# Kernel optimization log

Hardware: AMD Instinct MI355X
Metric: run time of the kernel (lower is better)

Reference implementation:

```python
import jax, jax.numpy as jnp
import numpy as np

C_CURV = 1.0  # hyperbolic curvature (init kwarg c)
EPS = 1e-7


def _to_ball(v, max_norm=0.8):
    # rescale rows to lie strictly inside the unit Poincare ball
    n = jnp.linalg.norm(v, axis=-1, keepdims=True)
    return v * (max_norm / (n + 1.0))


def setup_inputs() -> dict:
    key = jax.random.key(0)
    k1, k2 = jax.random.split(key)
    B, C, D = 32768, 2048, 512
    z_mix = _to_ball(jax.random.normal(k1, (B, D), dtype=jnp.float32))
    prototypes = _to_ball(jax.random.normal(k2, (C, D), dtype=jnp.float32))
    repel_margin = jnp.float32(2.0)
    return {"z_mix": z_mix, "prototypes": prototypes, "repel_margin": repel_margin}


def dist_matrix(x, y, c):
    # Poincare-ball pairwise distance (arccosh form):
    # d(x,y) = arccosh(1 + 2c||x-y||^2 / ((1-c||x||^2)(1-c||y||^2))) / sqrt(c)
    x2 = jnp.sum(x * x, axis=-1)            # (B,)
    y2 = jnp.sum(y * y, axis=-1)            # (C,)
    xy = jnp.einsum('bd,cd->bc', x, y)      # (B, C)
    sqdist = jnp.maximum(x2[:, None] + y2[None, :] - 2.0 * xy, 0.0)
    denom = (1.0 - c * x2)[:, None] * (1.0 - c * y2)[None, :]
    arg = 1.0 + 2.0 * c * sqdist / jnp.maximum(denom, EPS)
    return jnp.arccosh(jnp.maximum(arg, 1.0 + EPS)) / jnp.sqrt(c)


def reference(z_mix, prototypes, repel_margin):
    dist2proto = dist_matrix(z_mix, prototypes, C_CURV)   # (B, C)
    min_dist = jnp.min(dist2proto, axis=1)                # (B,)
    return jnp.mean(jax.nn.relu(repel_margin - min_dist))
```

## Files before the change

kernel.cpp:

```cpp
#include <hip/hip_runtime.h>
#include <stdint.h>

#define EPS_F 1e-7f

typedef float f32x4 __attribute__((ext_vector_type(4)));
typedef int   v8i   __attribute__((ext_vector_type(8)));

union A32 { uint4 u4[2]; v8i v; };

__device__ __forceinline__ unsigned cvt4(float a, float b, float c, float d) {
  int v = __builtin_amdgcn_cvt_pk_fp8_f32(a, b, 0, false);
  return (unsigned)__builtin_amdgcn_cvt_pk_fp8_f32(c, d, v, true);
}

#define MFMA128(A, B, C) __builtin_amdgcn_mfma_scale_f32_16x16x128_f8f6f4( \
    (A), (B), (C), 0, 0, 0, 0x7F7F7F7F, 0, 0x7F7F7F7F)


__global__ __launch_bounds__(256) void prep_kernel(
    const float* __restrict__ protos, uint8_t* __restrict__ wsB,
    float* __restrict__ y2a, float* __restrict__ rya,
    float* __restrict__ out) {
  const int lane = threadIdx.x & 63;
  const int w    = threadIdx.x >> 6;
  const int c    = blockIdx.x * 4 + w;
  const int g    = c >> 4, cl = c & 15;
  const float4* p = (const float4*)(protos + (size_t)c * 512 + lane * 8);
  float4 f0 = p[0], f1 = p[1];
  float s = f0.x*f0.x + f0.y*f0.y + f0.z*f0.z + f0.w*f0.w
          + f1.x*f1.x + f1.y*f1.y + f1.z*f1.z + f1.w*f1.w;
#pragma unroll
  for (int off = 32; off > 0; off >>= 1) s += __shfl_xor(s, off, 64);
  if (lane == 0) { y2a[c] = s; rya[c] = 1.f / (1.f - s); }
  unsigned ux = cvt4(f0.x, f0.y, f0.z, f0.w);
  unsigned uy = cvt4(f1.x, f1.y, f1.z, f1.w);
  const int kb = lane >> 4, kg = (lane >> 2) & 3, bo = lane & 3;
  size_t ri  = (size_t)(g * 4 + kb) * 64 + kg * 16 + cl;
  size_t off = ri * 16 + (size_t)(bo & 1) * 8 + (size_t)(bo >> 1) * (512u * 1024u);
  *(uint2*)(wsB + off) = make_uint2(ux, uy);
  if (blockIdx.x == 0 && threadIdx.x == 0) out[0] = 0.f;
}

__global__ __launch_bounds__(512, 1) void gemm_min_kernel(
    const float* __restrict__ z, const uint8_t* __restrict__ wsB,
    const float* __restrict__ y2a, const float* __restrict__ rya,
    const float* __restrict__ marg, float* __restrict__ out) {
  __shared__ uint4 As2[2048];
  __shared__ float x2s[64];
  __shared__ float rxs[64];
  __shared__ float minbuf[64][8];

  const int tid  = threadIdx.x;
  const int lane = tid & 63;
  const int w    = tid >> 6;
  const int q    = lane >> 4;
  const int l15  = lane & 15;
  const size_t rowbase = (size_t)blockIdx.x * 64;

  const uint4* BLo = (const uint4*)wsB;
  const uint4* BHi = BLo + 32768;

  A32 Bp0[2], Bp1[2];
#pragma unroll
  for (int i = 0; i < 2; ++i) {
    size_t r0 = (size_t)(w * 64 + i) * 64 + lane;
    Bp0[i].u4[0] = BLo[r0];       Bp0[i].u4[1] = BHi[r0];
    Bp1[i].u4[0] = BLo[r0 + 256]; Bp1[i].u4[1] = BHi[r0 + 256];
  }

  {
    const int c4 = lane & 3;
    const int m  = lane >> 2;
    const float* zb = z + (rowbase + w * 8) * 512 + lane * 4;
    float p0 = 0.f, p1 = 0.f, p2 = 0.f, p3 = 0.f,
          p4 = 0.f, p5 = 0.f, p6 = 0.f, p7 = 0.f;
#pragma unroll
    for (int ss = 0; ss < 4; ++ss) {
      float4 f0 = *(const float4*)(zb + (2 * ss + 0) * 512);
      float4 f1 = *(const float4*)(zb + (2 * ss + 0) * 512 + 256);
      float4 f2 = *(const float4*)(zb + (2 * ss + 1) * 512);
      float4 f3 = *(const float4*)(zb + (2 * ss + 1) * 512 + 256);
      float sa = f0.x*f0.x + f0.y*f0.y + f0.z*f0.z + f0.w*f0.w
               + f1.x*f1.x + f1.y*f1.y + f1.z*f1.z + f1.w*f1.w;
      float sb = f2.x*f2.x + f2.y*f2.y + f2.z*f2.z + f2.w*f2.w
               + f3.x*f3.x + f3.y*f3.y + f3.z*f3.z + f3.w*f3.w;
      if (ss == 0) { p0 += sa; p1 += sb; }
      if (ss == 1) { p2 += sa; p3 += sb; }
      if (ss == 2) { p4 += sa; p5 += sb; }
      if (ss == 3) { p6 += sa; p7 += sb; }
      unsigned v0 = cvt4(f0.x, f0.y, f0.z, f0.w);
      unsigned v1 = cvt4(f1.x, f1.y, f1.z, f1.w);
      unsigned v2 = cvt4(f2.x, f2.y, f2.z, f2.w);
      unsigned v3 = cvt4(f3.x, f3.y, f3.z, f3.w);
      unsigned t;
      t = (unsigned)__shfl_xor((int)((c4 & 1) ? v0 : v1), 1, 64);
      if (c4 & 1) v0 = t; else v1 = t;
      t = (unsigned)__shfl_xor((int)((c4 & 1) ? v2 : v3), 1, 64);
      if (c4 & 1) v2 = t; else v3 = t;
      t = (unsigned)__shfl_xor((int)((c4 & 2) ? v0 : v2), 2, 64);
      if (c4 & 2) v0 = t; else v2 = t;
      t = (unsigned)__shfl_xor((int)((c4 & 2) ? v1 : v3), 2, 64);
      if (c4 & 2) v1 = t; else v3 = t;
      int K   = ((c4 & 1) << 8) + (m << 4);
      int kb  = K >> 7;
      int kg  = (K >> 5) & 3;
      int pl  = (K >> 4) & 1;
      int r15 = ((w & 1) << 3) + 2 * ss + (c4 >> 1);
      int rf  = w >> 1;
      int ri  = pl * 1024 + (kb * 4 + rf) * 64 + kg * 16 + r15;
      As2[ri] = make_uint4(v0, v1, v2, v3);
    }
    float pr[8] = {p0, p1, p2, p3, p4, p5, p6, p7};
#pragma unroll
    for (int i = 0; i < 8; ++i) {
      float v = pr[i];
#pragma unroll
      for (int off = 32; off > 0; off >>= 1) v += __shfl_xor(v, off, 64);
      if (lane == 0) { x2s[w * 8 + i] = v; rxs[w * 8 + i] = 1.f / (1.f - v); }
    }
  }
  __syncthreads();

  float x2r[4][4];
#pragma unroll
  for (int rf = 0; rf < 4; ++rf) {
    float4 x4 = *(const float4*)&x2s[rf * 16 + q * 4];
    x2r[rf][0] = x4.x; x2r[rf][1] = x4.y; x2r[rf][2] = x4.z; x2r[rf][3] = x4.w;
  }

  float tmin[4][4];
#pragma unroll
  for (int rf = 0; rf < 4; ++rf)
#pragma unroll
    for (int r = 0; r < 4; ++r) tmin[rf][r] = 3.4e38f;

  const float* y2p = y2a + w * 256 + l15;
  const float* ryp = rya + w * 256 + l15;

#pragma clang loop unroll(disable)
  for (int s = 0; s < 8; ++s) {
    f32x4 acc[4][2];
#pragma unroll
    for (int rf = 0; rf < 4; ++rf) {
      f32x4 z4 = {0.f, 0.f, 0.f, 0.f};
      acc[rf][0] = z4; acc[rf][1] = z4;
    }
    float y2v0 = y2p[s * 32],      ryv0 = ryp[s * 32];
    float y2v1 = y2p[s * 32 + 16], ryv1 = ryp[s * 32 + 16];

#pragma unroll
    for (int kb = 0; kb < 4; ++kb) {
#pragma unroll
      for (int rf = 0; rf < 4; ++rf) {
        A32 a;
        int ri = (kb * 4 + rf) * 64 + lane;
        a.u4[0] = As2[ri];
        a.u4[1] = As2[1024 + ri];
        acc[rf][0] = MFMA128(a.v, Bp0[kb & 1].v, acc[rf][0]);
        acc[rf][1] = MFMA128(a.v, Bp1[kb & 1].v, acc[rf][1]);
      }
      {
        int ip = s * 4 + kb + 2;
        size_t r0 = (size_t)(w * 64 + (ip >> 2) * 8 + (ip & 3)) * 64 + lane;
        Bp0[kb & 1].u4[0] = BLo[r0];       Bp0[kb & 1].u4[1] = BHi[r0];
        Bp1[kb & 1].u4[0] = BLo[r0 + 256]; Bp1[kb & 1].u4[1] = BHi[r0 + 256];
      }
    }

#pragma unroll
    for (int rf = 0; rf < 4; ++rf) {
#pragma unroll
      for (int r = 0; r < 4; ++r) {
        float xv = x2r[rf][r];
        float u0 = fmaxf(fmaf(-2.f, acc[rf][0][r], xv + y2v0), 0.f) * ryv0;
        float u1 = fmaxf(fmaf(-2.f, acc[rf][1][r], xv + y2v1), 0.f) * ryv1;
        tmin[rf][r] = fminf(tmin[rf][r], fminf(u0, u1));
      }
    }
  }

#pragma unroll
  for (int rf = 0; rf < 4; ++rf) {
#pragma unroll
    for (int r = 0; r < 4; ++r) {
      float v = tmin[rf][r];
      v = fminf(v, __shfl_xor(v, 1, 64));
      v = fminf(v, __shfl_xor(v, 2, 64));
      v = fminf(v, __shfl_xor(v, 4, 64));
      v = fminf(v, __shfl_xor(v, 8, 64));
      if (l15 == 0) minbuf[rf * 16 + q * 4 + r][w] = v;
    }
  }
  __syncthreads();

  if (w == 0) {
    float m = minbuf[lane][0];
#pragma unroll
    for (int i = 1; i < 8; ++i) m = fminf(m, minbuf[lane][i]);
    float t = m * rxs[lane];
    float arg = fmaxf(fmaf(2.f, t, 1.f), 1.f + EPS_F);
    float contrib = fmaxf(marg[0] - acoshf(arg), 0.f);
#pragma unroll
    for (int off = 32; off > 0; off >>= 1) contrib += __shfl_xor(contrib, off, 64);
    if (lane == 0) atomicAdd(out, contrib * (1.0f / 32768.f));
  }
}

extern "C" void kernel_launch(void* const* d_in, const int* in_sizes, int n_in,
                              void* d_out, int out_size, void* d_ws, size_t ws_size,
                              hipStream_t stream) {
  const float* z      = (const float*)d_in[0];
  const float* protos = (const float*)d_in[1];
  const float* marg   = (const float*)d_in[2];
  float* out = (float*)d_out;
  uint8_t* wsB = (uint8_t*)d_ws;
  float* y2a = (float*)((char*)d_ws + (1 << 20) + 192 * 1024);
  float* rya = y2a + 2048;

  prep_kernel<<<512, 256, 0, stream>>>(protos, wsB, y2a, rya, out);
  gemm_min_kernel<<<512, 512, 0, stream>>>(z, wsB, y2a, rya, marg, out);
}
```

Measured before the change: 135.3 us.

## Double row tile per block to 128 and halve waves per block

```diff
diff --git a/kernel.cpp b/kernel.cpp
--- a/kernel.cpp
+++ b/kernel.cpp
@@ -41,21 +41,21 @@
   if (blockIdx.x == 0 && threadIdx.x == 0) out[0] = 0.f;
 }
 
-__global__ __launch_bounds__(512, 1) void gemm_min_kernel(
+__global__ __launch_bounds__(256, 1) void gemm_min_kernel(
     const float* __restrict__ z, const uint8_t* __restrict__ wsB,
     const float* __restrict__ y2a, const float* __restrict__ rya,
     const float* __restrict__ marg, float* __restrict__ out) {
-  __shared__ uint4 As2[2048];
-  __shared__ float x2s[64];
-  __shared__ float rxs[64];
-  __shared__ float minbuf[64][8];
+  __shared__ uint4 As2[4096];
+  __shared__ float x2s[128];
+  __shared__ float rxs[128];
+  __shared__ float minbuf[128][4];
 
   const int tid  = threadIdx.x;
   const int lane = tid & 63;
   const int w    = tid >> 6;
   const int q    = lane >> 4;
   const int l15  = lane & 15;
-  const size_t rowbase = (size_t)blockIdx.x * 64;
+  const size_t rowbase = (size_t)blockIdx.x * 128;
 
   const uint4* BLo = (const uint4*)wsB;
   const uint4* BHi = BLo + 32768;
@@ -63,7 +63,7 @@
   A32 Bp0[2], Bp1[2];
 #pragma unroll
   for (int i = 0; i < 2; ++i) {
-    size_t r0 = (size_t)(w * 64 + i) * 64 + lane;
+    size_t r0 = (size_t)(w * 128 + i) * 64 + lane;
     Bp0[i].u4[0] = BLo[r0];       Bp0[i].u4[1] = BHi[r0];
     Bp1[i].u4[0] = BLo[r0 + 256]; Bp1[i].u4[1] = BHi[r0 + 256];
   }
@@ -71,11 +71,9 @@
   {
     const int c4 = lane & 3;
     const int m  = lane >> 2;
-    const float* zb = z + (rowbase + w * 8) * 512 + lane * 4;
-    float p0 = 0.f, p1 = 0.f, p2 = 0.f, p3 = 0.f,
-          p4 = 0.f, p5 = 0.f, p6 = 0.f, p7 = 0.f;
-#pragma unroll
-    for (int ss = 0; ss < 4; ++ss) {
+    const float* zb = z + (rowbase + w * 32) * 512 + lane * 4;
+#pragma unroll
+    for (int ss = 0; ss < 16; ++ss) {
       float4 f0 = *(const float4*)(zb + (2 * ss + 0) * 512);
       float4 f1 = *(const float4*)(zb + (2 * ss + 0) * 512 + 256);
       float4 f2 = *(const float4*)(zb + (2 * ss + 1) * 512);
@@ -84,10 +82,16 @@
                + f1.x*f1.x + f1.y*f1.y + f1.z*f1.z + f1.w*f1.w;
       float sb = f2.x*f2.x + f2.y*f2.y + f2.z*f2.z + f2.w*f2.w
                + f3.x*f3.x + f3.y*f3.y + f3.z*f3.z + f3.w*f3.w;
-      if (ss == 0) { p0 += sa; p1 += sb; }
-      if (ss == 1) { p2 += sa; p3 += sb; }
-      if (ss == 2) { p4 += sa; p5 += sb; }
-      if (ss == 3) { p6 += sa; p7 += sb; }
+#pragma unroll
+      for (int off = 32; off > 0; off >>= 1) {
+        sa += __shfl_xor(sa, off, 64);
+        sb += __shfl_xor(sb, off, 64);
+      }
+      if (lane == 0) {
+        int r0 = w * 32 + 2 * ss;
+        x2s[r0] = sa;     rxs[r0] = 1.f / (1.f - sa);
+        x2s[r0 + 1] = sb; rxs[r0 + 1] = 1.f / (1.f - sb);
+      }
       unsigned v0 = cvt4(f0.x, f0.y, f0.z, f0.w);
       unsigned v1 = cvt4(f1.x, f1.y, f1.z, f1.w);
       unsigned v2 = cvt4(f2.x, f2.y, f2.z, f2.w);
@@ -105,43 +109,36 @@
       int kb  = K >> 7;
       int kg  = (K >> 5) & 3;
       int pl  = (K >> 4) & 1;
-      int r15 = ((w & 1) << 3) + 2 * ss + (c4 >> 1);
-      int rf  = w >> 1;
-      int ri  = pl * 1024 + (kb * 4 + rf) * 64 + kg * 16 + r15;
+      int rr  = 2 * ss + (c4 >> 1);
+      int rf  = 2 * w + (rr >> 4);
+      int r15 = rr & 15;
+      int ri  = pl * 2048 + (kb * 8 + rf) * 64 + kg * 16 + r15;
       As2[ri] = make_uint4(v0, v1, v2, v3);
     }
-    float pr[8] = {p0, p1, p2, p3, p4, p5, p6, p7};
-#pragma unroll
-    for (int i = 0; i < 8; ++i) {
-      float v = pr[i];
-#pragma unroll
-      for (int off = 32; off > 0; off >>= 1) v += __shfl_xor(v, off, 64);
-      if (lane == 0) { x2s[w * 8 + i] = v; rxs[w * 8 + i] = 1.f / (1.f - v); }
-    }
   }
   __syncthreads();
 
-  float x2r[4][4];
-#pragma unroll
-  for (int rf = 0; rf < 4; ++rf) {
+  float x2r[8][4];
+#pragma unroll
+  for (int rf = 0; rf < 8; ++rf) {
     float4 x4 = *(const float4*)&x2s[rf * 16 + q * 4];
     x2r[rf][0] = x4.x; x2r[rf][1] = x4.y; x2r[rf][2] = x4.z; x2r[rf][3] = x4.w;
   }
 
-  float tmin[4][4];
-#pragma unroll
-  for (int rf = 0; rf < 4; ++rf)
+  float tmin[8][4];
+#pragma unroll
+  for (int rf = 0; rf < 8; ++rf)
 #pragma unroll
     for (int r = 0; r < 4; ++r) tmin[rf][r] = 3.4e38f;
 
-  const float* y2p = y2a + w * 256 + l15;
-  const float* ryp = rya + w * 256 + l15;
+  const float* y2p = y2a + w * 512 + l15;
+  const float* ryp = rya + w * 512 + l15;
 
 #pragma clang loop unroll(disable)
-  for (int s = 0; s < 8; ++s) {
-    f32x4 acc[4][2];
-#pragma unroll
-    for (int rf = 0; rf < 4; ++rf) {
+  for (int s = 0; s < 16; ++s) {
+    f32x4 acc[8][2];
+#pragma unroll
+    for (int rf = 0; rf < 8; ++rf) {
       f32x4 z4 = {0.f, 0.f, 0.f, 0.f};
       acc[rf][0] = z4; acc[rf][1] = z4;
     }
@@ -150,25 +147,27 @@
 
 #pragma unroll
     for (int kb = 0; kb < 4; ++kb) {
-#pragma unroll
-      for (int rf = 0; rf < 4; ++rf) {
-        A32 a;
-        int ri = (kb * 4 + rf) * 64 + lane;
-        a.u4[0] = As2[ri];
-        a.u4[1] = As2[1024 + ri];
-        acc[rf][0] = MFMA128(a.v, Bp0[kb & 1].v, acc[rf][0]);
-        acc[rf][1] = MFMA128(a.v, Bp1[kb & 1].v, acc[rf][1]);
-      }
+      v8i bv0 = Bp0[kb & 1].v;
+      v8i bv1 = Bp1[kb & 1].v;
       {
         int ip = s * 4 + kb + 2;
-        size_t r0 = (size_t)(w * 64 + (ip >> 2) * 8 + (ip & 3)) * 64 + lane;
+        size_t r0 = (size_t)(w * 128 + (ip >> 2) * 8 + (ip & 3)) * 64 + lane;
         Bp0[kb & 1].u4[0] = BLo[r0];       Bp0[kb & 1].u4[1] = BHi[r0];
         Bp1[kb & 1].u4[0] = BLo[r0 + 256]; Bp1[kb & 1].u4[1] = BHi[r0 + 256];
       }
-    }
-
-#pragma unroll
-    for (int rf = 0; rf < 4; ++rf) {
+#pragma unroll
+      for (int rf = 0; rf < 8; ++rf) {
+        A32 a;
+        int ri = (kb * 8 + rf) * 64 + lane;
+        a.u4[0] = As2[ri];
+        a.u4[1] = As2[2048 + ri];
+        acc[rf][0] = MFMA128(a.v, bv0, acc[rf][0]);
+        acc[rf][1] = MFMA128(a.v, bv1, acc[rf][1]);
+      }
+    }
+
+#pragma unroll
+    for (int rf = 0; rf < 8; ++rf) {
 #pragma unroll
       for (int r = 0; r < 4; ++r) {
         float xv = x2r[rf][r];
@@ -180,7 +179,7 @@
   }
 
 #pragma unroll
-  for (int rf = 0; rf < 4; ++rf) {
+  for (int rf = 0; rf < 8; ++rf) {
 #pragma unroll
     for (int r = 0; r < 4; ++r) {
       float v = tmin[rf][r];
@@ -193,11 +192,11 @@
   }
   __syncthreads();
 
-  if (w == 0) {
-    float m = minbuf[lane][0];
-#pragma unroll
-    for (int i = 1; i < 8; ++i) m = fminf(m, minbuf[lane][i]);
-    float t = m * rxs[lane];
+  if (w < 2) {
+    int row = w * 64 + lane;
+    float m = fminf(fminf(minbuf[row][0], minbuf[row][1]),
+                    fminf(minbuf[row][2], minbuf[row][3]));
+    float t = m * rxs[row];
     float arg = fmaxf(fmaf(2.f, t, 1.f), 1.f + EPS_F);
     float contrib = fmaxf(marg[0] - acoshf(arg), 0.f);
 #pragma unroll
@@ -218,5 +217,5 @@
   float* rya = y2a + 2048;
 
   prep_kernel<<<512, 256, 0, stream>>>(protos, wsB, y2a, rya, out);
-  gemm_min_kernel<<<512, 512, 0, stream>>>(z, wsB, y2a, rya, marg, out);
-}
+  gemm_min_kernel<<<256, 256, 0, stream>>>(z, wsB, y2a, rya, marg, out);
+}
```

Result: no change. 135.8 us (+0.4%).
